# Performance work log

Measured on AMD Instinct MI355X. Metric: run time of the kernel, lower is better.

## Reference

```python
import jax, jax.numpy as jnp
import numpy as np

N_NODES = 40000
N_EDGES = 640000
HIDDEN = 128
NUM_RBF = 50
CUTOFF = 10.0


def setup_inputs() -> dict:
    key = jax.random.key(0)
    ks = jax.random.split(key, 8)
    s = 1.0 / np.sqrt(HIDDEN)
    sf = 1.0 / np.sqrt(NUM_RBF)
    return {
        "x": jax.random.normal(ks[0], (N_NODES, HIDDEN), dtype=jnp.float32),
        "edge_index": jax.random.randint(ks[1], (2, N_EDGES), 0, N_NODES, dtype=jnp.int64),
        "edge_weight": jax.random.uniform(ks[2], (N_EDGES,), dtype=jnp.float32) * CUTOFF,
        "edge_attr": jax.random.normal(ks[3], (N_EDGES, NUM_RBF), dtype=jnp.float32),
        "W_f1": jax.random.normal(ks[4], (NUM_RBF, HIDDEN), dtype=jnp.float32) * sf,
        "b_f1": jnp.zeros((HIDDEN,), dtype=jnp.float32),
        "W_f2": jax.random.normal(ks[5], (HIDDEN, HIDDEN), dtype=jnp.float32) * s,
        "b_f2": jnp.zeros((HIDDEN,), dtype=jnp.float32),
        "W_in": jax.random.normal(ks[6], (HIDDEN, HIDDEN), dtype=jnp.float32) * s,
        "W_out": jax.random.normal(ks[7], (HIDDEN, HIDDEN), dtype=jnp.float32) * s,
        "b_out": jnp.zeros((HIDDEN,), dtype=jnp.float32),
        "W_lin": jax.random.normal(jax.random.fold_in(key, 7), (HIDDEN, HIDDEN), dtype=jnp.float32) * s,
        "b_lin": jnp.zeros((HIDDEN,), dtype=jnp.float32),
    }


def reference(x, edge_index, edge_weight, edge_attr,
              W_f1, b_f1, W_f2, b_f2, W_in, W_out, b_out, W_lin, b_lin):
    src = edge_index[0]
    dst = edge_index[1]
    n_nodes = x.shape[0]
    # filter network: MLP on RBF-expanded distances, modulated by cosine cutoff
    C = 0.5 * (jnp.cos(edge_weight * (jnp.pi / CUTOFF)) + 1.0)  # [E]
    Wf = jnp.tanh(edge_attr @ W_f1 + b_f1) @ W_f2 + b_f2        # [E, H]
    Wf = Wf * C[:, None]
    # cfconv: project, gather, filter-multiply, scatter-add, project
    h = x @ W_in                                                 # [N, H] (no bias)
    msg = h[src] * Wf                                            # [E, H]
    agg = jax.ops.segment_sum(msg, dst, num_segments=n_nodes)   # [N, H]
    out = agg @ W_out + b_out
    # interaction block tail: activation + linear
    out = jnp.tanh(out)
    return out @ W_lin + b_lin
```

## Files before the change

kernel.cpp:

```cpp
#include <hip/hip_runtime.h>
#include <hip/hip_bf16.h>

#define N_NODES 40000
#define N_EDGES 640000
#define HIDDEN  128
#define NUM_RBF 50
#define NBLK_SCAN 157

typedef __attribute__((ext_vector_type(8))) short bf16x8;
typedef __attribute__((ext_vector_type(4))) float f32x4;

#define WAVE_FENCE() do { asm volatile("" ::: "memory"); \
                          __builtin_amdgcn_sched_barrier(0); } while (0)

__device__ __forceinline__ short f2bf(float f) {
  __hip_bfloat16 h = __float2bfloat16(f);
  return (short)__builtin_bit_cast(unsigned short, h);
}
__device__ __forceinline__ float bf2f(unsigned short u) {
  unsigned int v = ((unsigned int)u) << 16;
  return __builtin_bit_cast(float, v);
}
__device__ __forceinline__ float bflo(unsigned int u) {
  return __builtin_bit_cast(float, u << 16);
}
__device__ __forceinline__ float bfhi(unsigned int u) {
  return __builtin_bit_cast(float, u & 0xffff0000u);
}
__device__ __forceinline__ unsigned int pack2bf(float a, float b) {
  return (unsigned int)(unsigned short)f2bf(a) |
         ((unsigned int)(unsigned short)f2bf(b) << 16);
}

__device__ __forceinline__ float fast_tanh(float x) {
  float e = __expf(2.0f * x);
  return 1.0f - 2.0f * __builtin_amdgcn_rcpf(e + 1.0f);
}

__device__ __forceinline__ f32x4 mfma16(bf16x8 a, bf16x8 b, f32x4 c) {
  return __builtin_amdgcn_mfma_f32_16x16x32_bf16(a, b, c, 0, 0, 0);
}

__device__ __forceinline__ bf16x8 load8_f32_bf16(const float* p) {
  const float4 v0 = ((const float4*)p)[0];
  const float4 v1 = ((const float4*)p)[1];
  bf16x8 r;
  r[0] = f2bf(v0.x); r[1] = f2bf(v0.y); r[2] = f2bf(v0.z); r[3] = f2bf(v0.w);
  r[4] = f2bf(v1.x); r[5] = f2bf(v1.y); r[6] = f2bf(v1.z); r[7] = f2bf(v1.w);
  return r;
}

__global__ __launch_bounds__(256) void hist_kernel(const int* __restrict__ ei,
                                                   int* __restrict__ hist) {
  int e = blockIdx.x * 256 + threadIdx.x;
  if (e < N_EDGES) atomicAdd(&hist[ei[N_EDGES + e]], 1);
}

__global__ __launch_bounds__(256) void scan1_kernel(const int* __restrict__ hist,
                                                    int* __restrict__ tmp,
                                                    int* __restrict__ bsum) {
  __shared__ int ls[256];
  const int t = threadIdx.x;
  const int i = blockIdx.x * 256 + t;
  int v = (i < N_NODES) ? hist[i] : 0;
  ls[t] = v;
  __syncthreads();
  for (int off = 1; off < 256; off <<= 1) {
    int u = (t >= off) ? ls[t - off] : 0;
    __syncthreads();
    ls[t] += u;
    __syncthreads();
  }
  if (i < N_NODES) tmp[i] = ls[t];
  if (t == 255) bsum[blockIdx.x] = ls[255];
}

__global__ __launch_bounds__(256) void scan2_kernel(const int* __restrict__ bsum,
                                                    int* __restrict__ bpfx,
                                                    int* __restrict__ row_start) {
  __shared__ int ls[256];
  const int t = threadIdx.x;
  int v = (t < NBLK_SCAN) ? bsum[t] : 0;
  ls[t] = v;
  __syncthreads();
  for (int off = 1; off < 256; off <<= 1) {
    int u = (t >= off) ? ls[t - off] : 0;
    __syncthreads();
    ls[t] += u;
    __syncthreads();
  }
  if (t < NBLK_SCAN) bpfx[t] = ls[t] - v;
  if (t == 255) row_start[N_NODES] = ls[255];
}

__global__ __launch_bounds__(256) void scan3_kernel(const int* __restrict__ hist,
                                                    const int* __restrict__ tmp,
                                                    const int* __restrict__ bpfx,
                                                    int* __restrict__ row_start,
                                                    int* __restrict__ cursor) {
  const int i = blockIdx.x * 256 + threadIdx.x;
  if (i < N_NODES) {
    int rs = tmp[i] - hist[i] + bpfx[blockIdx.x];
    row_start[i] = rs;
    cursor[i] = rs;
  }
}

__global__ __launch_bounds__(256) void perm_kernel(const int* __restrict__ ei,
                                                   int* __restrict__ cursor,
                                                   int2* __restrict__ epk) {
  int e = blockIdx.x * 256 + threadIdx.x;
  if (e < N_EDGES) {
    int dst = ei[N_EDGES + e];
    int pos = atomicAdd(&cursor[dst], 1);
    epk[pos] = make_int2(e, ei[e]);
  }
}

__global__ __launch_bounds__(256) void hproj_kernel(
    const float* __restrict__ x, const float* __restrict__ W_in,
    unsigned short* __restrict__ hb)
{
  __shared__ __align__(16) unsigned short sWt[128 * 136];
  const int tid = threadIdx.x, wave = tid >> 6, lane = tid & 63;
  const int ln = lane & 15, grp = lane >> 4;
  const int r0 = blockIdx.x * 64;

  for (int idx = tid; idx < 128 * 128; idx += 256) {
    int k = idx >> 7, c = idx & 127;
    sWt[c * 136 + k] = f2bf(W_in[idx]);
  }
  __syncthreads();

  const size_t r = (size_t)r0 + wave * 16 + ln;
  f32x4 acc[8];
#pragma unroll
  for (int ct = 0; ct < 8; ++ct) acc[ct] = (f32x4){0.f, 0.f, 0.f, 0.f};
#pragma unroll
  for (int ks = 0; ks < 4; ++ks) {
    bf16x8 a = load8_f32_bf16(&x[r * 128 + ks * 32 + grp * 8]);
#pragma unroll
    for (int ct = 0; ct < 8; ++ct) {
      bf16x8 b = *(const bf16x8*)&sWt[(ct * 16 + ln) * 136 + ks * 32 + grp * 8];
      acc[ct] = mfma16(a, b, acc[ct]);
    }
  }
#pragma unroll
  for (int ct = 0; ct < 8; ++ct) {
#pragma unroll
    for (int i = 0; i < 4; ++i) {
      hb[(size_t)(r0 + wave * 16 + grp * 4 + i) * 128 + ct * 16 + ln] =
          (unsigned short)f2bf(acc[ct][i]);
    }
  }
}

__global__ __launch_bounds__(1024) void edgeagg_kernel(
    const float* __restrict__ edge_attr,
    const float* __restrict__ edge_weight,
    const int*  __restrict__ row_start,
    const int2* __restrict__ epk,
    const unsigned int* __restrict__ hb32,
    const float* __restrict__ W_f1, const float* __restrict__ b_f1,
    const float* __restrict__ W_f2, const float* __restrict__ b_f2,
    float* __restrict__ aggf)
{
  __shared__ __align__(16) unsigned short sW1t[128 * 72];
  __shared__ __align__(16) unsigned short sW2t[128 * 136];
  __shared__ __align__(16) unsigned short sT[256 * 136];
  __shared__ float sb1[128], sb2[128];

  const int tid = threadIdx.x, wave = tid >> 6, lane = tid & 63;
  const int ln = lane & 15, grp = lane >> 4;

  for (int idx = tid; idx < 128 * 64; idx += 1024) {
    int k = idx >> 7, c = idx & 127;
    sW1t[c * 72 + k] = (k < NUM_RBF) ? f2bf(W_f1[k * 128 + c]) : (short)0;
  }
  for (int idx = tid; idx < 128 * 128; idx += 1024) {
    int k = idx >> 7, c = idx & 127;
    sW2t[c * 136 + k] = f2bf(W_f2[idx]);
  }
  if (tid < 128) { sb1[tid] = b_f1[tid]; sb2[tid] = b_f2[tid]; }
  __syncthreads();

  const int gw = blockIdx.x * 16 + wave;
  const int nw = gridDim.x * 16;
  const int nGroups = N_NODES / 4;

  for (int ng = gw; ng < nGroups; ng += nw) {
    const int n0 = ng * 4;
    const int rs0 = row_start[n0],     rs1 = row_start[n0 + 1];
    const int rs2 = row_start[n0 + 2], rs3 = row_start[n0 + 3];
    const int rs4 = row_start[n0 + 4];

    float ax = 0.f, ay = 0.f;
    int cur = 0;
    int nb = rs1;

    for (int gb = rs0; gb < rs4; gb += 16) {
      const int lim = (rs4 - gb < 16) ? (rs4 - gb) : 16;

      unsigned int hv[16];
#pragma unroll
      for (int j = 0; j < 16; ++j) {
        int s = gb + j; if (s >= rs4) s = rs4 - 1;
        int src = epk[s].y;
        hv[j] = hb32[(size_t)src * 64 + lane];
      }

      int sl = gb + ln; if (sl >= rs4) sl = rs4 - 1;
      const int eA = epk[sl].x;
      const float Cw =
          0.5f * (__cosf(edge_weight[eA] * 0.31415926535f) + 1.0f);

      const float* ap = edge_attr + (size_t)eA * NUM_RBF;
      bf16x8 a0, a1;
      {
        const float2* p = (const float2*)(ap + grp * 8);
        float2 v0 = p[0], v1 = p[1], v2 = p[2], v3 = p[3];
        a0[0] = f2bf(v0.x); a0[1] = f2bf(v0.y); a0[2] = f2bf(v1.x); a0[3] = f2bf(v1.y);
        a0[4] = f2bf(v2.x); a0[5] = f2bf(v2.y); a0[6] = f2bf(v3.x); a0[7] = f2bf(v3.y);
      }
      a1 = (bf16x8){0, 0, 0, 0, 0, 0, 0, 0};
      if (grp < 2) {
        const float2* p = (const float2*)(ap + 32 + grp * 8);
        float2 v0 = p[0], v1 = p[1], v2 = p[2], v3 = p[3];
        a1[0] = f2bf(v0.x); a1[1] = f2bf(v0.y); a1[2] = f2bf(v1.x); a1[3] = f2bf(v1.y);
        a1[4] = f2bf(v2.x); a1[5] = f2bf(v2.y); a1[6] = f2bf(v3.x); a1[7] = f2bf(v3.y);
      } else if (grp == 2) {
        const float2* p = (const float2*)(ap + 48);
        float2 v0 = p[0];
        a1[0] = f2bf(v0.x); a1[1] = f2bf(v0.y);
      }

#pragma unroll
      for (int ct = 0; ct < 8; ++ct) {
        f32x4 z = {0.f, 0.f, 0.f, 0.f};
        int c = ct * 16 + ln;
        bf16x8 b0 = *(const bf16x8*)&sW1t[c * 72 + grp * 8];
        bf16x8 b1 = *(const bf16x8*)&sW1t[c * 72 + 32 + grp * 8];
        z = mfma16(a0, b0, z);
        z = mfma16(a1, b1, z);
        float bias = sb1[c];
#pragma unroll
        for (int i = 0; i < 4; ++i) {
          int rl = wave * 16 + grp * 4 + i;
          sT[rl * 136 + c] = (unsigned short)f2bf(fast_tanh(z[i] + bias));
        }
      }
      WAVE_FENCE();

      bf16x8 af[4];
#pragma unroll
      for (int ks = 0; ks < 4; ++ks)
        af[ks] = *(const bf16x8*)&sT[(wave * 16 + ln) * 136 + ks * 32 + grp * 8];
      WAVE_FENCE();
#pragma unroll
      for (int ct = 0; ct < 8; ++ct) {
        f32x4 z = {0.f, 0.f, 0.f, 0.f};
        int c = ct * 16 + ln;
#pragma unroll
        for (int ks = 0; ks < 4; ++ks) {
          bf16x8 b = *(const bf16x8*)&sW2t[c * 136 + ks * 32 + grp * 8];
          z = mfma16(af[ks], b, z);
        }
        float bias = sb2[c];
#pragma unroll
        for (int i = 0; i < 4; ++i) {
          int rl = wave * 16 + grp * 4 + i;
          sT[rl * 136 + c] = (unsigned short)f2bf(z[i] + bias);
        }
      }
      WAVE_FENCE();

#pragma unroll
      for (int j = 0; j < 16; ++j) {
        if (j < lim) {
          while (cur < 4 && gb + j == nb) {
            ((float2*)aggf)[(size_t)(n0 + cur) * 64 + lane] =
                make_float2(ax, ay);
            ax = 0.f; ay = 0.f;
            ++cur;
            nb = (cur == 1) ? rs2 : (cur == 2) ? rs3 : rs4;
          }
          unsigned int w = *(const unsigned int*)&sT[(wave * 16 + j) * 136 + lane * 2];
          float C = __shfl(Cw, j, 64);
          ax = fmaf(C * bflo(w), bflo(hv[j]), ax);
          ay = fmaf(C * bfhi(w), bfhi(hv[j]), ay);
        }
      }
      WAVE_FENCE();
    }

    while (cur < 4) {
      ((float2*)aggf)[(size_t)(n0 + cur) * 64 + lane] = make_float2(ax, ay);
      ax = 0.f; ay = 0.f;
      ++cur;
    }
  }
}

__global__ __launch_bounds__(256) void tail_kernel(
    const float* agg,
    const float* __restrict__ W_out, const float* __restrict__ b_out,
    const float* __restrict__ W_lin, const float* __restrict__ b_lin,
    float* out)
{
  __shared__ __align__(16) unsigned short sWo[128 * 136];
  __shared__ __align__(16) unsigned short sWl[128 * 136];
  __shared__ __align__(16) unsigned short sT[64 * 136];
  __shared__ float sbo[128], sbl[128];
  const int tid = threadIdx.x, wave = tid >> 6, lane = tid & 63;
  const int ln = lane & 15, grp = lane >> 4;
  const int r0 = blockIdx.x * 64;

  for (int idx = tid; idx < 128 * 128; idx += 256) {
    int k = idx >> 7, c = idx & 127;
    sWo[c * 136 + k] = f2bf(W_out[idx]);
    sWl[c * 136 + k] = f2bf(W_lin[idx]);
  }
  if (tid < 128) { sbo[tid] = b_out[tid]; sbl[tid] = b_lin[tid]; }
  __syncthreads();

  const size_t r = (size_t)r0 + wave * 16 + ln;
  f32x4 acc[8];
#pragma unroll
  for (int ct = 0; ct < 8; ++ct) acc[ct] = (f32x4){0.f, 0.f, 0.f, 0.f};
#pragma unroll
  for (int ks = 0; ks < 4; ++ks) {
    bf16x8 a = load8_f32_bf16(&agg[r * 128 + ks * 32 + grp * 8]);
#pragma unroll
    for (int ct = 0; ct < 8; ++ct) {
      bf16x8 b = *(const bf16x8*)&sWo[(ct * 16 + ln) * 136 + ks * 32 + grp * 8];
      acc[ct] = mfma16(a, b, acc[ct]);
    }
  }
#pragma unroll
  for (int ct = 0; ct < 8; ++ct) {
    int c = ct * 16 + ln;
    float bias = sbo[c];
#pragma unroll
    for (int i = 0; i < 4; ++i) {
      int rl = wave * 16 + grp * 4 + i;
      sT[rl * 136 + c] = f2bf(fast_tanh(acc[ct][i] + bias));
    }
  }
  __syncthreads();

  bf16x8 af[4];
#pragma unroll
  for (int ks = 0; ks < 4; ++ks)
    af[ks] = *(const bf16x8*)&sT[(wave * 16 + ln) * 136 + ks * 32 + grp * 8];
  f32x4 acc2[8];
#pragma unroll
  for (int ct = 0; ct < 8; ++ct) {
    f32x4 z = {0.f, 0.f, 0.f, 0.f};
    int c = ct * 16 + ln;
#pragma unroll
    for (int ks = 0; ks < 4; ++ks) {
      bf16x8 b = *(const bf16x8*)&sWl[c * 136 + ks * 32 + grp * 8];
      z = mfma16(af[ks], b, z);
    }
    acc2[ct] = z;
  }
  __syncthreads();
#pragma unroll
  for (int ct = 0; ct < 8; ++ct) {
    int c = ct * 16 + ln;
    float bias = sbl[c];
#pragma unroll
    for (int i = 0; i < 4; ++i) {
      out[(size_t)(r0 + wave * 16 + grp * 4 + i) * 128 + c] = acc2[ct][i] + bias;
    }
  }
}

__global__ __launch_bounds__(256, 2) void edge_kernel(
    const float* __restrict__ edge_attr,
    const int*   __restrict__ edge_index,
    const float* __restrict__ edge_weight,
    const float* __restrict__ W_f1, const float* __restrict__ b_f1,
    const float* __restrict__ W_f2, const float* __restrict__ b_f2,
    const unsigned short* __restrict__ hb, float* __restrict__ agg)
{
  __shared__ __align__(16) unsigned short sW1t[128 * 72];
  __shared__ __align__(16) unsigned short sW2t[128 * 136];
  __shared__ __align__(16) unsigned short sT[64 * 136];
  __shared__ float sb1[128], sb2[128], sC[64];
  __shared__ int sSrc[64], sDst[64];

  const int tid = threadIdx.x, wave = tid >> 6, lane = tid & 63;
  const int ln = lane & 15, grp = lane >> 4;

  for (int idx = tid; idx < 128 * 64; idx += 256) {
    int k = idx >> 7, c = idx & 127;
    sW1t[c * 72 + k] = (k < NUM_RBF) ? f2bf(W_f1[k * 128 + c]) : (short)0;
  }
  for (int idx = tid; idx < 128 * 128; idx += 256) {
    int k = idx >> 7, c = idx & 127;
    sW2t[c * 136 + k] = f2bf(W_f2[idx]);
  }
  if (tid < 128) { sb1[tid] = b_f1[tid]; sb2[tid] = b_f2[tid]; }

  const int nTiles = N_EDGES / 64;
  for (int tile = blockIdx.x; tile < nTiles; tile += gridDim.x) {
    const int e0 = tile * 64;
    for (int idx = tid; idx < 64 * NUM_RBF; idx += 256) {
      int e = idx / NUM_RBF, k = idx - e * NUM_RBF;
      sT[e * 136 + k] = f2bf(edge_attr[(size_t)e0 * NUM_RBF + idx]);
    }
    for (int idx = tid; idx < 64 * 14; idx += 256) {
      int e = idx / 14, k = NUM_RBF + (idx - (idx / 14) * 14);
      sT[e * 136 + k] = 0;
    }
    if (tid < 64) {
      int e = e0 + tid;
      sC[tid] = 0.5f * (__cosf(edge_weight[e] * 0.31415926535f) + 1.0f);
      sSrc[tid] = edge_index[e];
      sDst[tid] = edge_index[N_EDGES + e];
    }
    __syncthreads();

    const int erow = wave * 16 + ln;
    bf16x8 a0 = *(const bf16x8*)&sT[erow * 136 + grp * 8];
    bf16x8 a1 = *(const bf16x8*)&sT[erow * 136 + 32 + grp * 8];
    __syncthreads();

    f32x4 acc[8];
#pragma unroll
    for (int ct = 0; ct < 8; ++ct) {
      f32x4 z = {0.f, 0.f, 0.f, 0.f};
      int c = ct * 16 + ln;
      bf16x8 b0 = *(const bf16x8*)&sW1t[c * 72 + grp * 8];
      bf16x8 b1 = *(const bf16x8*)&sW1t[c * 72 + 32 + grp * 8];
      z = mfma16(a0, b0, z);
      z = mfma16(a1, b1, z);
      acc[ct] = z;
    }
#pragma unroll
    for (int ct = 0; ct < 8; ++ct) {
      int c = ct * 16 + ln;
      float bias = sb1[c];
#pragma unroll
      for (int i = 0; i < 4; ++i) {
        int el = wave * 16 + grp * 4 + i;
        sT[el * 136 + c] = f2bf(fast_tanh(acc[ct][i] + bias));
      }
    }
    __syncthreads();

    bf16x8 af[4];
#pragma unroll
    for (int ks = 0; ks < 4; ++ks)
      af[ks] = *(const bf16x8*)&sT[erow * 136 + ks * 32 + grp * 8];
    f32x4 acc2[8];
#pragma unroll
    for (int ct = 0; ct < 8; ++ct) {
      f32x4 z = {0.f, 0.f, 0.f, 0.f};
      int c = ct * 16 + ln;
#pragma unroll
      for (int ks = 0; ks < 4; ++ks) {
        bf16x8 b = *(const bf16x8*)&sW2t[c * 136 + ks * 32 + grp * 8];
        z = mfma16(af[ks], b, z);
      }
      acc2[ct] = z;
    }
#pragma unroll
    for (int ct = 0; ct < 8; ++ct) {
      int c = ct * 16 + ln;
      float bias = sb2[c];
#pragma unroll
      for (int i = 0; i < 4; ++i) {
        int el = wave * 16 + grp * 4 + i;
        float wf = (acc2[ct][i] + bias) * sC[el];
        float m = bf2f(hb[(size_t)sSrc[el] * 128 + c]) * wf;
        atomicAdd(&agg[(size_t)sDst[el] * 128 + c], m);
      }
    }
    __syncthreads();
  }
}

extern "C" void kernel_launch(void* const* d_in, const int* in_sizes, int n_in,
                              void* d_out, int out_size, void* d_ws, size_t ws_size,
                              hipStream_t stream) {
  const float* x     = (const float*)d_in[0];
  const int*   ei    = (const int*)d_in[1];
  const float* ew    = (const float*)d_in[2];
  const float* ea    = (const float*)d_in[3];
  const float* W_f1  = (const float*)d_in[4];
  const float* b_f1  = (const float*)d_in[5];
  const float* W_f2  = (const float*)d_in[6];
  const float* b_f2  = (const float*)d_in[7];
  const float* W_in  = (const float*)d_in[8];
  const float* W_out = (const float*)d_in[9];
  const float* b_out = (const float*)d_in[10];
  const float* W_lin = (const float*)d_in[11];
  const float* b_lin = (const float*)d_in[12];

  const size_t HB_B  = (size_t)N_NODES * HIDDEN * 2;
  const size_t I_B   = (size_t)N_NODES * 4;
  const size_t RS_B  = ((size_t)(N_NODES + 1) * 4 + 15) & ~(size_t)15;
  const size_t SB_B  = 1024;
  const size_t EPK_B = (size_t)N_EDGES * 8;
  const size_t NEED = HB_B + I_B + RS_B + I_B + I_B + SB_B + SB_B + EPK_B;

  char* ws = (char*)d_ws;
  unsigned short* hb = (unsigned short*)ws;

  if (ws_size >= NEED) {
    char* q = ws + HB_B;
    int* hist      = (int*)q;                  q += I_B;
    int* row_start = (int*)q;                  q += RS_B;
    int* cursor    = (int*)q;                  q += I_B;
    int* tmp       = (int*)q;                  q += I_B;
    int* bsum      = (int*)q;                  q += SB_B;
    int* bpfx      = (int*)q;                  q += SB_B;
    int2* epk      = (int2*)q;

    hipMemsetAsync(hist, 0, I_B, stream);
    hist_kernel<<<(N_EDGES + 255) / 256, 256, 0, stream>>>(ei, hist);
    scan1_kernel<<<NBLK_SCAN, 256, 0, stream>>>(hist, tmp, bsum);
    scan2_kernel<<<1, 256, 0, stream>>>(bsum, bpfx, row_start);
    scan3_kernel<<<NBLK_SCAN, 256, 0, stream>>>(hist, tmp, bpfx, row_start, cursor);
    perm_kernel<<<(N_EDGES + 255) / 256, 256, 0, stream>>>(ei, cursor, epk);
    hproj_kernel<<<N_NODES / 64, 256, 0, stream>>>(x, W_in, hb);
    edgeagg_kernel<<<256, 1024, 0, stream>>>(ea, ew, row_start, epk,
                                             (const unsigned int*)hb,
                                             W_f1, b_f1, W_f2, b_f2,
                                             (float*)d_out);
    tail_kernel<<<N_NODES / 64, 256, 0, stream>>>((const float*)d_out,
                                                  W_out, b_out, W_lin, b_lin,
                                                  (float*)d_out);
  } else {
    float* agg = (float*)(ws + HB_B);
    hipMemsetAsync(agg, 0, (size_t)N_NODES * HIDDEN * 4, stream);
    hproj_kernel<<<N_NODES / 64, 256, 0, stream>>>(x, W_in, hb);
    edge_kernel<<<512, 256, 0, stream>>>(ea, ei, ew, W_f1, b_f1, W_f2, b_f2, hb, agg);
    tail_kernel<<<N_NODES / 64, 256, 0, stream>>>(agg, W_out, b_out, W_lin, b_lin,
                                                  (float*)d_out);
  }
}
```

Before: 226.2 us.

## Pre-permute edge attributes into dst-sorted bf16 layout before aggregation

A new prep kernel reads the fp32 edge_attr rows coalesced, packs them to bf16 padded to 64 elements, and scatters them into dst-sorted order. The permutation kernel now also stores sorted source indices and precomputes the cosine cutoff per sorted position. The aggregation kernel can then read contiguous bf16 attribute rows, cutoff values and source indices instead of doing indirect fp32 gathers and converting each time. The cost is an extra kernel pass that writes about 80 MB and an extra scattered write of edge_attr, which may outweigh the savings. The fallback path's atomicAdd also switches to an edge_index lookup.

```diff
diff --git a/kernel.cpp b/kernel.cpp
--- a/kernel.cpp
+++ b/kernel.cpp
@@ -106,14 +106,52 @@
   }
 }
 
-__global__ __launch_bounds__(256) void perm_kernel(const int* __restrict__ ei,
-                                                   int* __restrict__ cursor,
-                                                   int2* __restrict__ epk) {
+__global__ __launch_bounds__(256) void perm_kernel(
+    const int* __restrict__ ei, const float* __restrict__ ew,
+    int* __restrict__ cursor,
+    int* __restrict__ posOf, int* __restrict__ srcSorted,
+    float* __restrict__ Carr) {
   int e = blockIdx.x * 256 + threadIdx.x;
   if (e < N_EDGES) {
     int dst = ei[N_EDGES + e];
     int pos = atomicAdd(&cursor[dst], 1);
-    epk[pos] = make_int2(e, ei[e]);
+    posOf[e] = pos;
+    srcSorted[pos] = ei[e];
+    Carr[pos] = 0.5f * (__cosf(ew[e] * 0.31415926535f) + 1.0f);
+  }
+}
+
+__global__ __launch_bounds__(256) void prep_kernel(
+    const float* __restrict__ edge_attr,
+    const int* __restrict__ posOf,
+    unsigned int* __restrict__ eab32)
+{
+  __shared__ unsigned int sS[4 * 16 * 32];
+  const int wave = threadIdx.x >> 6, lane = threadIdx.x & 63;
+  unsigned int* slab = &sS[wave * 512];
+
+  const int nChunks = N_EDGES / 16;
+  for (int chunk = blockIdx.x * 4 + wave; chunk < nChunks;
+       chunk += gridDim.x * 4) {
+    const int e0 = chunk * 16;
+    for (int idx = lane; idx < 16 * 25; idx += 64) {
+      int e = idx / 25, u = idx - e * 25;
+      float2 v = ((const float2*)edge_attr)[(size_t)e0 * 25 + idx];
+      slab[e * 32 + u] = pack2bf(v.x, v.y);
+    }
+    for (int idx = lane; idx < 16 * 7; idx += 64) {
+      int e = idx / 7, u = 25 + (idx - e * 7);
+      slab[e * 32 + u] = 0;
+    }
+    WAVE_FENCE();
+
+#pragma unroll
+    for (int jj = 0; jj < 16; jj += 2) {
+      int j = jj + (lane >> 5);
+      int pos = posOf[e0 + j];
+      eab32[(size_t)pos * 32 + (lane & 31)] = slab[j * 32 + (lane & 31)];
+    }
+    WAVE_FENCE();
   }
 }
 
@@ -156,10 +194,10 @@
 }
 
 __global__ __launch_bounds__(1024) void edgeagg_kernel(
-    const float* __restrict__ edge_attr,
-    const float* __restrict__ edge_weight,
-    const int*  __restrict__ row_start,
-    const int2* __restrict__ epk,
+    const unsigned short* __restrict__ eab,
+    const int*   __restrict__ srcSorted,
+    const float* __restrict__ Carr,
+    const int*   __restrict__ row_start,
     const unsigned int* __restrict__ hb32,
     const float* __restrict__ W_f1, const float* __restrict__ b_f1,
     const float* __restrict__ W_f2, const float* __restrict__ b_f2,
@@ -205,34 +243,15 @@
 #pragma unroll
       for (int j = 0; j < 16; ++j) {
         int s = gb + j; if (s >= rs4) s = rs4 - 1;
-        int src = epk[s].y;
+        int src = srcSorted[s];
         hv[j] = hb32[(size_t)src * 64 + lane];
       }
 
       int sl = gb + ln; if (sl >= rs4) sl = rs4 - 1;
-      const int eA = epk[sl].x;
-      const float Cw =
-          0.5f * (__cosf(edge_weight[eA] * 0.31415926535f) + 1.0f);
-
-      const float* ap = edge_attr + (size_t)eA * NUM_RBF;
-      bf16x8 a0, a1;
-      {
-        const float2* p = (const float2*)(ap + grp * 8);
-        float2 v0 = p[0], v1 = p[1], v2 = p[2], v3 = p[3];
-        a0[0] = f2bf(v0.x); a0[1] = f2bf(v0.y); a0[2] = f2bf(v1.x); a0[3] = f2bf(v1.y);
-        a0[4] = f2bf(v2.x); a0[5] = f2bf(v2.y); a0[6] = f2bf(v3.x); a0[7] = f2bf(v3.y);
-      }
-      a1 = (bf16x8){0, 0, 0, 0, 0, 0, 0, 0};
-      if (grp < 2) {
-        const float2* p = (const float2*)(ap + 32 + grp * 8);
-        float2 v0 = p[0], v1 = p[1], v2 = p[2], v3 = p[3];
-        a1[0] = f2bf(v0.x); a1[1] = f2bf(v0.y); a1[2] = f2bf(v1.x); a1[3] = f2bf(v1.y);
-        a1[4] = f2bf(v2.x); a1[5] = f2bf(v2.y); a1[6] = f2bf(v3.x); a1[7] = f2bf(v3.y);
-      } else if (grp == 2) {
-        const float2* p = (const float2*)(ap + 48);
-        float2 v0 = p[0];
-        a1[0] = f2bf(v0.x); a1[1] = f2bf(v0.y);
-      }
+      const float Cw = Carr[sl];
+      const unsigned short* ar = eab + (size_t)sl * 64;
+      bf16x8 a0 = *(const bf16x8*)(ar + grp * 8);
+      bf16x8 a1 = *(const bf16x8*)(ar + 32 + grp * 8);
 
 #pragma unroll
       for (int ct = 0; ct < 8; ++ct) {
@@ -475,7 +494,7 @@
         int el = wave * 16 + grp * 4 + i;
         float wf = (acc2[ct][i] + bias) * sC[el];
         float m = bf2f(hb[(size_t)sSrc[el] * 128 + c]) * wf;
-        atomicAdd(&agg[(size_t)sDst[el] * 128 + c], m);
+        atomicAdd(&agg[(size_t)edge_index[N_EDGES + e0 + el] * 128 + c], m);
       }
     }
     __syncthreads();
@@ -503,8 +522,10 @@
   const size_t I_B   = (size_t)N_NODES * 4;
   const size_t RS_B  = ((size_t)(N_NODES + 1) * 4 + 15) & ~(size_t)15;
   const size_t SB_B  = 1024;
-  const size_t EPK_B = (size_t)N_EDGES * 8;
-  const size_t NEED = HB_B + I_B + RS_B + I_B + I_B + SB_B + SB_B + EPK_B;
+  const size_t POS_B = (size_t)N_EDGES * 4;
+  const size_t EAB_B = (size_t)N_EDGES * 64 * 2;
+  const size_t NEED = HB_B + I_B + RS_B + I_B + I_B + SB_B + SB_B +
+                      3 * POS_B + EAB_B;
 
   char* ws = (char*)d_ws;
   unsigned short* hb = (unsigned short*)ws;
@@ -517,16 +538,21 @@
     int* tmp       = (int*)q;                  q += I_B;
     int* bsum      = (int*)q;                  q += SB_B;
     int* bpfx      = (int*)q;                  q += SB_B;
-    int2* epk      = (int2*)q;
+    int* posOf     = (int*)q;                  q += POS_B;
+    int* srcSorted = (int*)q;                  q += POS_B;
+    float* Carr    = (float*)q;                q += POS_B;
+    unsigned short* eab = (unsigned short*)q;
 
     hipMemsetAsync(hist, 0, I_B, stream);
     hist_kernel<<<(N_EDGES + 255) / 256, 256, 0, stream>>>(ei, hist);
     scan1_kernel<<<NBLK_SCAN, 256, 0, stream>>>(hist, tmp, bsum);
     scan2_kernel<<<1, 256, 0, stream>>>(bsum, bpfx, row_start);
     scan3_kernel<<<NBLK_SCAN, 256, 0, stream>>>(hist, tmp, bpfx, row_start, cursor);
-    perm_kernel<<<(N_EDGES + 255) / 256, 256, 0, stream>>>(ei, cursor, epk);
+    perm_kernel<<<(N_EDGES + 255) / 256, 256, 0, stream>>>(ei, ew, cursor,
+                                                           posOf, srcSorted, Carr);
+    prep_kernel<<<1024, 256, 0, stream>>>(ea, posOf, (unsigned int*)eab);
     hproj_kernel<<<N_NODES / 64, 256, 0, stream>>>(x, W_in, hb);
-    edgeagg_kernel<<<256, 1024, 0, stream>>>(ea, ew, row_start, epk,
+    edgeagg_kernel<<<256, 1024, 0, stream>>>(eab, srcSorted, Carr, row_start,
                                              (const unsigned int*)hb,
                                              W_f1, b_f1, W_f2, b_f2,
                                              (float*)d_out);
```

Result: slower. 301.8 us (+33.5%).

## Use atomic ticket scheduling and precompute cutoff into sorted SoA edge arrays

Applied to the files above, without the earlier changes.

Replaces the static strided assignment of node groups to waves with a dynamic work queue driven by an atomic ticket counter, so waves that land on light groups keep picking up work. The perm kernel now stores the original edge id, source node and cosine cutoff value in three separate arrays in sorted order. This removes the scattered edge_weight gather and the cosine evaluation from the aggregation kernel and turns the packed int2 reads into coalesced int reads. The cost is an extra memset, one atomic per group, and an extra 2.5 MB cutoff array written and then read back.

```diff
diff --git a/kernel.cpp b/kernel.cpp
--- a/kernel.cpp
+++ b/kernel.cpp
@@ -106,14 +106,18 @@
   }
 }
 
-__global__ __launch_bounds__(256) void perm_kernel(const int* __restrict__ ei,
-                                                   int* __restrict__ cursor,
-                                                   int2* __restrict__ epk) {
+__global__ __launch_bounds__(256) void perm_kernel(
+    const int* __restrict__ ei, const float* __restrict__ ew,
+    int* __restrict__ cursor,
+    int* __restrict__ eSorted, int* __restrict__ srcSorted,
+    float* __restrict__ Carr) {
   int e = blockIdx.x * 256 + threadIdx.x;
   if (e < N_EDGES) {
     int dst = ei[N_EDGES + e];
     int pos = atomicAdd(&cursor[dst], 1);
-    epk[pos] = make_int2(e, ei[e]);
+    eSorted[pos] = e;
+    srcSorted[pos] = ei[e];
+    Carr[pos] = 0.5f * (__cosf(ew[e] * 0.31415926535f) + 1.0f);
   }
 }
 
@@ -157,12 +161,14 @@
 
 __global__ __launch_bounds__(1024) void edgeagg_kernel(
     const float* __restrict__ edge_attr,
-    const float* __restrict__ edge_weight,
-    const int*  __restrict__ row_start,
-    const int2* __restrict__ epk,
+    const int*   __restrict__ eSorted,
+    const int*   __restrict__ srcSorted,
+    const float* __restrict__ Carr,
+    const int*   __restrict__ row_start,
     const unsigned int* __restrict__ hb32,
     const float* __restrict__ W_f1, const float* __restrict__ b_f1,
     const float* __restrict__ W_f2, const float* __restrict__ b_f2,
+    int* __restrict__ ticket,
     float* __restrict__ aggf)
 {
   __shared__ __align__(16) unsigned short sW1t[128 * 72];
@@ -184,11 +190,14 @@
   if (tid < 128) { sb1[tid] = b_f1[tid]; sb2[tid] = b_f2[tid]; }
   __syncthreads();
 
-  const int gw = blockIdx.x * 16 + wave;
-  const int nw = gridDim.x * 16;
   const int nGroups = N_NODES / 4;
 
-  for (int ng = gw; ng < nGroups; ng += nw) {
+  for (;;) {
+    int ng = 0;
+    if (lane == 0) ng = atomicAdd(ticket, 1);
+    ng = __shfl(ng, 0, 64);
+    if (ng >= nGroups) break;
+
     const int n0 = ng * 4;
     const int rs0 = row_start[n0],     rs1 = row_start[n0 + 1];
     const int rs2 = row_start[n0 + 2], rs3 = row_start[n0 + 3];
@@ -205,15 +214,13 @@
 #pragma unroll
       for (int j = 0; j < 16; ++j) {
         int s = gb + j; if (s >= rs4) s = rs4 - 1;
-        int src = epk[s].y;
+        int src = srcSorted[s];
         hv[j] = hb32[(size_t)src * 64 + lane];
       }
 
       int sl = gb + ln; if (sl >= rs4) sl = rs4 - 1;
-      const int eA = epk[sl].x;
-      const float Cw =
-          0.5f * (__cosf(edge_weight[eA] * 0.31415926535f) + 1.0f);
-
+      const int eA = eSorted[sl];
+      const float Cw = Carr[sl];
       const float* ap = edge_attr + (size_t)eA * NUM_RBF;
       bf16x8 a0, a1;
       {
@@ -503,8 +510,10 @@
   const size_t I_B   = (size_t)N_NODES * 4;
   const size_t RS_B  = ((size_t)(N_NODES + 1) * 4 + 15) & ~(size_t)15;
   const size_t SB_B  = 1024;
-  const size_t EPK_B = (size_t)N_EDGES * 8;
-  const size_t NEED = HB_B + I_B + RS_B + I_B + I_B + SB_B + SB_B + EPK_B;
+  const size_t POS_B = (size_t)N_EDGES * 4;
+  const size_t TK_B  = 64;
+  const size_t NEED = HB_B + I_B + RS_B + I_B + I_B + SB_B + SB_B +
+                      3 * POS_B + TK_B;
 
   char* ws = (char*)d_ws;
   unsigned short* hb = (unsigned short*)ws;
@@ -517,19 +526,25 @@
     int* tmp       = (int*)q;                  q += I_B;
     int* bsum      = (int*)q;                  q += SB_B;
     int* bpfx      = (int*)q;                  q += SB_B;
-    int2* epk      = (int2*)q;
+    int* eSorted   = (int*)q;                  q += POS_B;
+    int* srcSorted = (int*)q;                  q += POS_B;
+    float* Carr    = (float*)q;                q += POS_B;
+    int* ticket    = (int*)q;
 
     hipMemsetAsync(hist, 0, I_B, stream);
+    hipMemsetAsync(ticket, 0, TK_B, stream);
     hist_kernel<<<(N_EDGES + 255) / 256, 256, 0, stream>>>(ei, hist);
     scan1_kernel<<<NBLK_SCAN, 256, 0, stream>>>(hist, tmp, bsum);
     scan2_kernel<<<1, 256, 0, stream>>>(bsum, bpfx, row_start);
     scan3_kernel<<<NBLK_SCAN, 256, 0, stream>>>(hist, tmp, bpfx, row_start, cursor);
-    perm_kernel<<<(N_EDGES + 255) / 256, 256, 0, stream>>>(ei, cursor, epk);
+    perm_kernel<<<(N_EDGES + 255) / 256, 256, 0, stream>>>(ei, ew, cursor,
+                                                           eSorted, srcSorted, Carr);
     hproj_kernel<<<N_NODES / 64, 256, 0, stream>>>(x, W_in, hb);
-    edgeagg_kernel<<<256, 1024, 0, stream>>>(ea, ew, row_start, epk,
+    edgeagg_kernel<<<256, 1024, 0, stream>>>(ea, eSorted, srcSorted, Carr,
+                                             row_start,
                                              (const unsigned int*)hb,
                                              W_f1, b_f1, W_f2, b_f2,
-                                             (float*)d_out);
+                                             ticket, (float*)d_out);
     tail_kernel<<<N_NODES / 64, 256, 0, stream>>>((const float*)d_out,
                                                   W_out, b_out, W_lin, b_lin,
                                                   (float*)d_out);
```

Measured after the change: 314.5 us. 39.0% more time.
